# Optimization experiments

Measured on AMD Instinct MI355X. Metric: run time of the kernel, lower is better.

Reference implementation:

```python
import jax, jax.numpy as jnp
import numpy as np

B, N0, N1, FD, L, H = 4, 256, 256, 128, 3, 1
NG = N0 + N1            # nodes per graph
N = B * NG              # total nodes
EPS_BN = 1e-5
EPS_SM = 1e-16


def _build_edges():
    def perm_edges(n, off):
        idx = np.arange(n)
        a = np.repeat(idx, n); b = np.tile(idx, n)
        m = a != b
        return np.stack([a[m], b[m]]) + off
    e_intra = np.concatenate([perm_edges(N0, 0), perm_edges(N1, N0)], axis=1)
    a = np.arange(N0); b = np.arange(N0, N0 + N1)
    cross1 = np.stack([np.repeat(a, N1), np.tile(b, N0)])
    cross2 = np.stack([np.repeat(b, N0), np.tile(a, N1)])
    eg = np.concatenate([e_intra, cross1, cross2], axis=1)
    tg = np.concatenate([np.zeros(e_intra.shape[1], np.int32),
                         np.ones(cross1.shape[1] + cross2.shape[1], np.int32)])
    ei = np.concatenate([eg + g * NG for g in range(B)], axis=1).astype(np.int32)
    et = np.tile(tg, B).astype(np.int32)
    return jnp.asarray(ei), jnp.asarray(et)


def setup_inputs() -> dict:
    key = jax.random.key(0)
    ks = jax.random.split(key, 8)
    edge_index, edge_type = _build_edges()
    return {
        'desc0': jax.random.normal(ks[0], (B, FD, N0), jnp.float32),
        'desc1': jax.random.normal(ks[1], (B, FD, N1), jnp.float32),
        'W': jax.random.normal(ks[2], (L, 2, FD, H * FD), jnp.float32) * (1.0 / np.sqrt(FD)),
        'q': jax.random.normal(ks[3], (L, H * FD, H), jnp.float32) * 0.1,
        'k': jax.random.normal(ks[4], (L, H * FD, H), jnp.float32) * 0.1,
        'conv_b': jnp.zeros((L, FD), jnp.float32),
        'lin_W': jax.random.normal(ks[5], (L, FD, 2 * FD), jnp.float32) * (1.0 / np.sqrt(2 * FD)),
        'lin_b': jnp.zeros((L, FD), jnp.float32),
        'gamma': jnp.ones((L, FD), jnp.float32),
        'beta': jnp.zeros((L, FD), jnp.float32),
        'edge_index': edge_index,
        'edge_type': edge_type,
    }


def _forward(desc0, desc1, W, q, k, conv_b, lin_W, lin_b, gamma, beta, edge_index, edge_type):
    # x: [B, NG, FD] -> flattened batch graph [N, FD]
    x = jnp.concatenate([desc0, desc1], axis=2)        # [B, FD, NG]
    x = jnp.transpose(x, (0, 2, 1)).reshape(N, FD)
    src, dst = edge_index[0], edge_index[1]
    nlayers = W.shape[0]
    heads = q.shape[2]
    for l in range(nlayers):
        # relation-specific node projections (equiv to per-edge bmm with weight[edge_type])
        proj = jnp.einsum('nf,rfo->nro', x, W[l])       # [N, 2, H*FD]
        out_i = proj[dst, edge_type]                    # [E, H*FD]
        out_j = proj[src, edge_type]                    # [E, H*FD]
        alpha = jax.nn.leaky_relu(out_i @ q[l] + out_j @ k[l], 0.2)  # [E, H]
        # softmax over incoming edges of each destination node (across-relation)
        amax = jax.ops.segment_max(alpha, dst, num_segments=N)
        ex = jnp.exp(alpha - amax[dst])
        denom = jax.ops.segment_sum(ex, dst, num_segments=N)
        att = ex / (denom[dst] + EPS_SM)                # [E, H]
        msg = (att[:, :, None] * out_j.reshape(-1, heads, FD)).reshape(-1, heads * FD)
        agg = jax.ops.segment_sum(msg, dst, num_segments=N).reshape(N, heads, FD)
        m1 = jax.nn.relu(agg.mean(axis=1) + conv_b[l])  # concat=False -> mean over heads
        m2 = jnp.concatenate([x, m1], axis=1) @ lin_W[l].T + lin_b[l]
        mu = m2.mean(axis=0)
        var = ((m2 - mu) ** 2).mean(axis=0)             # biased var (BatchNorm training)
        m3 = (m2 - mu) / jnp.sqrt(var + EPS_BN) * gamma[l] + beta[l]
        x = x + m3
    x = x.reshape(B, NG, FD).transpose(0, 2, 1)         # [B, FD, NG]
    return x


def reference(desc0, desc1, W, q, k, conv_b, lin_W, lin_b, gamma, beta, edge_index, edge_type):
    x = _forward(desc0, desc1, W, q, k, conv_b, lin_W, lin_b, gamma, beta, edge_index, edge_type)
    return x[:, :, :N0], x[:, :, N0:]
```

## Files before the change

### kernel.cpp

```cpp
#include <hip/hip_runtime.h>

#define FD  128
#define NN  2048

#define OFF_X     0
#define OFF_PROJ  262144
#define OFF_QS    786432
#define OFF_KS    790528
#define OFF_SUMS  794624
#define OFF_LWT   800768
#define OFF_M2    899072

__device__ __forceinline__ int swizzle_n0(int bid) {
    int g    = (bid & 7) >> 1;
    int slot = ((bid >> 3) << 1) | (bid & 1);
    return g*512 + slot*4;
}

__device__ __forceinline__ void proj_qsks4(
    const float* __restrict__ W, const float* __restrict__ qv,
    const float* __restrict__ kv, float* __restrict__ ws,
    int l, int n0, int t, const float (*xs)[FD],
    float (*redp)[256], float* red)
{
    int kh = t >> 8, tp = t & 255;
    int rsel = tp >> 7, o = tp & 127;
    const float* Wl = W + ((size_t)(l*2 + rsel)*FD)*FD + o;
    float acc[4];
#pragma unroll
    for (int r = 0; r < 4; r++) acc[r] = 0.f;
    int kbase = kh * 64;
#pragma unroll
    for (int kk = 0; kk < 64; kk += 4) {
        int k4 = kbase + kk;
        float w0 = Wl[(k4+0)*FD], w1 = Wl[(k4+1)*FD];
        float w2 = Wl[(k4+2)*FD], w3 = Wl[(k4+3)*FD];
#pragma unroll
        for (int r = 0; r < 4; r++) {
            float4 xq = *(const float4*)&xs[r][k4];
            acc[r] += xq.x*w0 + xq.y*w1 + xq.z*w2 + xq.w*w3;
        }
    }
    if (kh == 1) {
#pragma unroll
        for (int r = 0; r < 4; r++) redp[r][tp] = acc[r];
    }
    __syncthreads();
    if (t < 256) {
#pragma unroll
        for (int r = 0; r < 4; r++) acc[r] += redp[r][tp];
#pragma unroll
        for (int r = 0; r < 4; r++)
            ws[OFF_PROJ + (size_t)(n0 + r)*256 + tp] = acc[r];

        float qq = qv[l*FD + o], kq = kv[l*FD + o];
        int lane = t & 63, w = t >> 6;
#pragma unroll
        for (int r = 0; r < 4; r++) {
            float vq = acc[r]*qq, vk = acc[r]*kq;
            for (int off = 32; off; off >>= 1) {
                vq += __shfl_xor(vq, off, 64);
                vk += __shfl_xor(vk, off, 64);
            }
            if (lane == 0) { red[w*8 + r*2] = vq; red[w*8 + r*2 + 1] = vk; }
        }
    }
    __syncthreads();
    if (t < 16) {
        int r = t & 3, rs = (t >> 2) & 1, wh = t >> 3;
        float v = red[(rs*2)*8 + r*2 + wh] + red[(rs*2 + 1)*8 + r*2 + wh];
        if (wh == 0) ws[OFF_QS + rs*NN + n0 + r] = v;
        else         ws[OFF_KS + rs*NN + n0 + r] = v;
    }
}

__global__ __launch_bounds__(512, 4) void k_pre(
    const float* __restrict__ d0, const float* __restrict__ d1,
    const float* __restrict__ W,  const float* __restrict__ qv,
    const float* __restrict__ kv, const float* __restrict__ linW,
    float* __restrict__ ws)
{
    int bid = blockIdx.x, t = threadIdx.x;
    if (bid >= 512) {
        if (bid < 536) {
            int vb = bid - 512;
#pragma unroll
            for (int i = 0; i < 8; i++) {
                int e = vb*4096 + i*512 + t;
                int l = e >> 15, rem = e & 32767;
                int o = rem >> 8, c = rem & 255;
                ws[OFF_LWT + l*32768 + c*FD + o] = linW[e];
            }
        } else {
            for (int i = t; i < 6144; i += 512) ws[OFF_SUMS + i] = 0.f;
        }
        return;
    }
    __shared__ __attribute__((aligned(16))) float xs[4][FD];
    __shared__ float redp[4][256];
    __shared__ float red[32];
    int n0 = swizzle_n0(bid);
    {
        int row = t >> 7, f = t & 127;
        int n = n0 + row, gg = n >> 9, ii = n & 511;
        float v = (ii < 256) ? d0[gg*32768 + f*256 + ii]
                             : d1[gg*32768 + f*256 + (ii - 256)];
        xs[row][f] = v;
        ws[OFF_X + (size_t)n*FD + f] = v;
    }
    __syncthreads();
    proj_qsks4(W, qv, kv, ws, 0, n0, t, xs, redp, red);
}

__global__ __launch_bounds__(512, 4) void k_bp(
    const float* __restrict__ W,     const float* __restrict__ qv,
    const float* __restrict__ kv,    const float* __restrict__ gamma,
    const float* __restrict__ beta,  float* __restrict__ ws, int l)
{
    __shared__ float scale[FD], shift[FD];
    __shared__ __attribute__((aligned(16))) float xs[4][FD];
    __shared__ float redp[4][256];
    __shared__ float red[32];
    int bid = blockIdx.x, t = threadIdx.x;
    int lp = l - 1;
    if (t < 128) {
        float s0 = 0.f, s1 = 0.f;
#pragma unroll
        for (int sl = 0; sl < 8; sl++) {
            s0 += ws[OFF_SUMS + lp*2048 + sl*256 + t];
            s1 += ws[OFF_SUMS + lp*2048 + sl*256 + 128 + t];
        }
        float mu  = s0 * (1.f/2048.f);
        float var = s1 * (1.f/2048.f) - mu*mu;
        float rs  = rsqrtf(var + 1e-5f);
        float gm  = gamma[lp*FD + t], bt = beta[lp*FD + t];
        scale[t] = gm * rs;
        shift[t] = bt - mu * gm * rs;
    }
    __syncthreads();
    int n0 = swizzle_n0(bid);
    {
        int row = t >> 7, f = t & 127;
        size_t e = (size_t)(n0 + row)*FD + f;
        float xv = ws[OFF_X + e] + ws[OFF_M2 + e]*scale[f] + shift[f];
        xs[row][f] = xv;
        ws[OFF_X + e] = xv;
    }
    __syncthreads();
    proj_qsks4(W, qv, kv, ws, l, n0, t, xs, redp, red);
}

__global__ __launch_bounds__(512, 4) void k_attn(
    const float* __restrict__ convb, const float* __restrict__ linb,
    float* __restrict__ ws, int l)
{
    __shared__ __attribute__((aligned(16))) float att[4*512];
    __shared__ __attribute__((aligned(16))) float redB[8*4*128];
    __shared__ __attribute__((aligned(16))) float cat[4*256];
    __shared__ float sml[4][2], sls[4][2];
    __shared__ float r1[FD], r2[FD];

    int bid = blockIdx.x, t = threadIdx.x;
    int dstbase = swizzle_n0(bid);
    int g = dstbase >> 9, dloc0 = dstbase & 511;
    int Gd = (dloc0 >= 256) ? 1 : 0;

    int f4 = t & 31, sq = t >> 5;
    int ts = (sq < 8) ? Gd : 1 - Gd;
    const float* P = ws + OFF_PROJ + (size_t)(g*512)*256 + ts*128 + f4*4;
    int s0 = sq * 32;
    float4 buf0[4], buf1[4], buf2[4];
#pragma unroll
    for (int u = 0; u < 4; u++) buf0[u] = *(const float4*)&P[(size_t)(s0+u)*256];
#pragma unroll
    for (int u = 0; u < 4; u++) buf1[u] = *(const float4*)&P[(size_t)(s0+4+u)*256];
    float xpre = ws[OFF_X + (size_t)(dstbase + (t >> 7))*FD + (t & 127)];
    float cb   = convb[l*FD + (t & 127)];
    float lb   = linb[l*FD + (t & 127)];

    {
        int w = t >> 6, p = t & 63;
        int d = w >> 1, h = w & 1;
        int dloc = dloc0 + d;
        float q0 = ws[OFF_QS + dstbase + d];
        float q1 = ws[OFF_QS + NN + dstbase + d];
        float sc[4];
#pragma unroll
        for (int j = 0; j < 4; j++) {
            int s = h*256 + p + j*64;
            int tss = (s < 256) ? Gd : 1 - Gd;
            float a = (tss ? q1 : q0) + ws[OFF_KS + tss*NN + g*512 + s];
            a = a > 0.f ? a : 0.2f*a;
            sc[j] = (s == dloc) ? -1e30f : a;
        }
        float lm = fmaxf(fmaxf(sc[0], sc[1]), fmaxf(sc[2], sc[3]));
        for (int off = 32; off; off >>= 1) lm = fmaxf(lm, __shfl_xor(lm, off, 64));
        float ex[4], lsum = 0.f;
#pragma unroll
        for (int j = 0; j < 4; j++) { ex[j] = __expf(sc[j] - lm); lsum += ex[j]; }
        for (int off = 32; off; off >>= 1) lsum += __shfl_xor(lsum, off, 64);
#pragma unroll
        for (int j = 0; j < 4; j++) att[d*512 + h*256 + p + j*64] = ex[j];
        if (p == 0) { sml[d][h] = lm; sls[d][h] = lsum; }
    }
    __syncthreads();
    {
        int d = t >> 7, s4 = (t & 127) * 4;
        int h = (s4 >= 256) ? 1 : 0;
        float m0 = sml[d][0], m1 = sml[d][1];
        float M = fmaxf(m0, m1);
        float denom = sls[d][0]*__expf(m0 - M) + sls[d][1]*__expf(m1 - M) + 1e-16f;
        float fac = __expf(sml[d][h] - M) / denom;
        float4 a4 = *(float4*)&att[d*512 + s4];
        a4.x *= fac; a4.y *= fac; a4.z *= fac; a4.w *= fac;
        *(float4*)&att[d*512 + s4] = a4;
        if (t < 128) r1[t] = 0.f;
        else if (t < 256) r2[t - 128] = 0.f;
    }
    __syncthreads();

    float acc[4][4];
#pragma unroll
    for (int d2 = 0; d2 < 4; d2++)
#pragma unroll
        for (int j = 0; j < 4; j++) acc[d2][j] = 0.f;
    {
#pragma unroll
        for (int ii = 0; ii < 8; ii++) {
            const float4* cur = (ii % 3 == 0) ? buf0 : (ii % 3 == 1) ? buf1 : buf2;
            float4* nxt = ((ii+2) % 3 == 0) ? buf0 : ((ii+2) % 3 == 1) ? buf1 : buf2;
            if (ii < 6) {
#pragma unroll
                for (int u = 0; u < 4; u++)
                    nxt[u] = *(const float4*)&P[(size_t)(s0 + (ii+2)*4 + u)*256];
            }
#pragma unroll
            for (int u = 0; u < 4; u++) {
                int s = s0 + ii*4 + u;
                float4 p4 = cur[u];
#pragma unroll
                for (int d2 = 0; d2 < 4; d2++) {
                    float b = att[d2*512 + s];
                    acc[d2][0] += b*p4.x; acc[d2][1] += b*p4.y;
                    acc[d2][2] += b*p4.z; acc[d2][3] += b*p4.w;
                }
            }
        }
    }
    if (sq >= 8) {
#pragma unroll
        for (int d2 = 0; d2 < 4; d2++)
            *(float4*)&redB[((sq - 8)*4 + d2)*128 + f4*4] =
                make_float4(acc[d2][0], acc[d2][1], acc[d2][2], acc[d2][3]);
    }
    __syncthreads();
    if (sq < 8) {
#pragma unroll
        for (int d2 = 0; d2 < 4; d2++) {
            float4 p4 = *(const float4*)&redB[(sq*4 + d2)*128 + f4*4];
            *(float4*)&redB[(sq*4 + d2)*128 + f4*4] =
                make_float4(acc[d2][0]+p4.x, acc[d2][1]+p4.y, acc[d2][2]+p4.z, acc[d2][3]+p4.w);
        }
    }
    __syncthreads();

    {
        int d2 = t >> 7, f = t & 127;
        float agg = 0.f;
#pragma unroll
        for (int cc = 0; cc < 8; cc++) agg += redB[(cc*4 + d2)*128 + f];
        float m1v = fmaxf(agg + cb, 0.f);
        cat[d2*256 + FD + f] = m1v;
        cat[d2*256 + f] = xpre;
    }
    __syncthreads();

#pragma unroll
    for (int d2 = 0; d2 < 4; d2++)
#pragma unroll
        for (int j = 0; j < 4; j++) acc[d2][j] = 0.f;
    {
        const float* lwt = ws + OFF_LWT + l*32768 + f4*4;
        int c0 = sq * 16;
#pragma unroll
        for (int u = 0; u < 4; u++) buf0[u] = *(const float4*)&lwt[(c0+u)*128];
#pragma unroll
        for (int u = 0; u < 4; u++) buf1[u] = *(const float4*)&lwt[(c0+4+u)*128];
#pragma unroll
        for (int ii = 0; ii < 4; ii++) {
            const float4* cur = (ii % 3 == 0) ? buf0 : (ii % 3 == 1) ? buf1 : buf2;
            float4* nxt = ((ii+2) % 3 == 0) ? buf0 : ((ii+2) % 3 == 1) ? buf1 : buf2;
            if (ii < 2) {
#pragma unroll
                for (int u = 0; u < 4; u++)
                    nxt[u] = *(const float4*)&lwt[(c0 + (ii+2)*4 + u)*128];
            }
#pragma unroll
            for (int u = 0; u < 4; u++) {
                int c = c0 + ii*4 + u;
                float4 w4 = cur[u];
#pragma unroll
                for (int d2 = 0; d2 < 4; d2++) {
                    float cv = cat[d2*256 + c];
                    acc[d2][0] += cv*w4.x; acc[d2][1] += cv*w4.y;
                    acc[d2][2] += cv*w4.z; acc[d2][3] += cv*w4.w;
                }
            }
        }
    }
    if (sq >= 8) {
#pragma unroll
        for (int d2 = 0; d2 < 4; d2++)
            *(float4*)&redB[((sq - 8)*4 + d2)*128 + f4*4] =
                make_float4(acc[d2][0], acc[d2][1], acc[d2][2], acc[d2][3]);
    }
    __syncthreads();
    if (sq < 8) {
#pragma unroll
        for (int d2 = 0; d2 < 4; d2++) {
            float4 p4 = *(const float4*)&redB[(sq*4 + d2)*128 + f4*4];
            *(float4*)&redB[(sq*4 + d2)*128 + f4*4] =
                make_float4(acc[d2][0]+p4.x, acc[d2][1]+p4.y, acc[d2][2]+p4.z, acc[d2][3]+p4.w);
        }
    }
    __syncthreads();

    {
        int d2 = t >> 7, o = t & 127;
        float m2v = lb;
#pragma unroll
        for (int cc = 0; cc < 8; cc++) m2v += redB[(cc*4 + d2)*128 + o];
        ws[OFF_M2 + (size_t)(dstbase + d2)*FD + o] = m2v;
        atomicAdd(&r1[o], m2v);
        atomicAdd(&r2[o], m2v*m2v);
    }
    __syncthreads();
    if (t < 128) {
        int slot = bid & 7;
        atomicAdd(&ws[OFF_SUMS + l*2048 + slot*256 + t],       r1[t]);
        atomicAdd(&ws[OFF_SUMS + l*2048 + slot*256 + 128 + t], r2[t]);
    }
}

__global__ __launch_bounds__(256) void k_bnout(
    const float* __restrict__ gamma, const float* __restrict__ beta,
    float* __restrict__ ws, float* __restrict__ out)
{
    __shared__ float scale[FD], shift[FD];
    int bid = blockIdx.x, t = threadIdx.x;
    if (t < 128) {
        float s0 = 0.f, s1 = 0.f;
#pragma unroll
        for (int sl = 0; sl < 8; sl++) {
            s0 += ws[OFF_SUMS + 2*2048 + sl*256 + t];
            s1 += ws[OFF_SUMS + 2*2048 + sl*256 + 128 + t];
        }
        float mu  = s0 * (1.f/2048.f);
        float var = s1 * (1.f/2048.f) - mu*mu;
        float rs  = rsqrtf(var + 1e-5f);
        float gm  = gamma[2*FD + t], bt = beta[2*FD + t];
        scale[t] = gm * rs;
        shift[t] = bt - mu * gm * rs;
    }
    __syncthreads();
#pragma unroll
    for (int i = 0; i < 2; i++) {
        int idx = bid*512 + i*256 + t;
        int f = idx & 127, n = idx >> 7;
        float v = ws[OFF_X + idx] + ws[OFF_M2 + idx]*scale[f] + shift[f];
        int gg = n >> 9, ii = n & 511;
        int off = (ii < 256) ? (gg*32768 + f*256 + ii)
                             : (131072 + gg*32768 + f*256 + (ii - 256));
        out[off] = v;
    }
}

extern "C" void kernel_launch(void* const* d_in, const int* in_sizes, int n_in,
                              void* d_out, int out_size, void* d_ws, size_t ws_size,
                              hipStream_t stream) {
    (void)in_sizes; (void)n_in; (void)out_size; (void)ws_size;
    const float* desc0 = (const float*)d_in[0];
    const float* desc1 = (const float*)d_in[1];
    const float* W     = (const float*)d_in[2];
    const float* q     = (const float*)d_in[3];
    const float* kk    = (const float*)d_in[4];
    const float* convb = (const float*)d_in[5];
    const float* linW  = (const float*)d_in[6];
    const float* linb  = (const float*)d_in[7];
    const float* gamma = (const float*)d_in[8];
    const float* beta  = (const float*)d_in[9];
    float* ws  = (float*)d_ws;
    float* out = (float*)d_out;

    hipLaunchKernelGGL(k_pre,  dim3(537), dim3(512), 0, stream, desc0, desc1, W, q, kk, linW, ws);
    hipLaunchKernelGGL(k_attn, dim3(512), dim3(512), 0, stream, convb, linb, ws, 0);
    hipLaunchKernelGGL(k_bp,   dim3(512), dim3(512), 0, stream, W, q, kk, gamma, beta, ws, 1);
    hipLaunchKernelGGL(k_attn, dim3(512), dim3(512), 0, stream, convb, linb, ws, 1);
    hipLaunchKernelGGL(k_bp,   dim3(512), dim3(512), 0, stream, W, q, kk, gamma, beta, ws, 2);
    hipLaunchKernelGGL(k_attn, dim3(512), dim3(512), 0, stream, convb, linb, ws, 2);
    hipLaunchKernelGGL(k_bnout, dim3(512), dim3(256), 0, stream, gamma, beta, ws, out);
}
```

Measured before the change: 153.4 us.

## Defer softmax normalization to accumulators, widen reduction buffer, hoist loads before barriers

The attention kernel no longer rescales the attention weights in shared memory in a separate pass. The per-half softmax factor is now applied to each thread's accumulators after the weighted sum. The two-step partial-sum reduction is replaced by all 16 groups writing to a doubled redB buffer, which removes several __syncthreads in both matmul phases. In k_bp and k_bnout, the global loads of x and m2 are hoisted above the BN-statistics barrier so their latency overlaps the stats computation. The cost is more shared memory per block, which could reduce occupancy, and a longer 16-way final sum.

```diff
diff --git a/kernel.cpp b/kernel.cpp
--- a/kernel.cpp
+++ b/kernel.cpp
@@ -123,6 +123,11 @@
     __shared__ float red[32];
     int bid = blockIdx.x, t = threadIdx.x;
     int lp = l - 1;
+    int n0 = swizzle_n0(bid);
+    int row = t >> 7, f = t & 127;
+    size_t e = (size_t)(n0 + row)*FD + f;
+    float xm  = ws[OFF_X + e];
+    float m2v = ws[OFF_M2 + e];
     if (t < 128) {
         float s0 = 0.f, s1 = 0.f;
 #pragma unroll
@@ -138,11 +143,8 @@
         shift[t] = bt - mu * gm * rs;
     }
     __syncthreads();
-    int n0 = swizzle_n0(bid);
-    {
-        int row = t >> 7, f = t & 127;
-        size_t e = (size_t)(n0 + row)*FD + f;
-        float xv = ws[OFF_X + e] + ws[OFF_M2 + e]*scale[f] + shift[f];
+    {
+        float xv = xm + m2v*scale[f] + shift[f];
         xs[row][f] = xv;
         ws[OFF_X + e] = xv;
     }
@@ -155,7 +157,7 @@
     float* __restrict__ ws, int l)
 {
     __shared__ __attribute__((aligned(16))) float att[4*512];
-    __shared__ __attribute__((aligned(16))) float redB[8*4*128];
+    __shared__ __attribute__((aligned(16))) float redB[16*4*128];
     __shared__ __attribute__((aligned(16))) float cat[4*256];
     __shared__ float sml[4][2], sls[4][2];
     __shared__ float r1[FD], r2[FD];
@@ -202,18 +204,8 @@
 #pragma unroll
         for (int j = 0; j < 4; j++) att[d*512 + h*256 + p + j*64] = ex[j];
         if (p == 0) { sml[d][h] = lm; sls[d][h] = lsum; }
-    }
-    __syncthreads();
-    {
-        int d = t >> 7, s4 = (t & 127) * 4;
-        int h = (s4 >= 256) ? 1 : 0;
-        float m0 = sml[d][0], m1 = sml[d][1];
-        float M = fmaxf(m0, m1);
-        float denom = sls[d][0]*__expf(m0 - M) + sls[d][1]*__expf(m1 - M) + 1e-16f;
-        float fac = __expf(sml[d][h] - M) / denom;
-        float4 a4 = *(float4*)&att[d*512 + s4];
-        a4.x *= fac; a4.y *= fac; a4.z *= fac; a4.w *= fac;
-        *(float4*)&att[d*512 + s4] = a4;
+        int d2 = t >> 7, f = t & 127;
+        cat[d2*256 + f] = xpre;
         if (t < 128) r1[t] = 0.f;
         else if (t < 256) r2[t - 128] = 0.f;
     }
@@ -246,21 +238,21 @@
                 }
             }
         }
-    }
-    if (sq >= 8) {
+        int h = (sq >= 8) ? 1 : 0;
+#pragma unroll
+        for (int d2 = 0; d2 < 4; d2++) {
+            float m0 = sml[d2][0], m1 = sml[d2][1];
+            float M = fmaxf(m0, m1);
+            float denom = sls[d2][0]*__expf(m0 - M) + sls[d2][1]*__expf(m1 - M)
+                        + 1e-16f;
+            float fac = __expf((h ? m1 : m0) - M) / denom;
+#pragma unroll
+            for (int j = 0; j < 4; j++) acc[d2][j] *= fac;
+        }
 #pragma unroll
         for (int d2 = 0; d2 < 4; d2++)
-            *(float4*)&redB[((sq - 8)*4 + d2)*128 + f4*4] =
+            *(float4*)&redB[(sq*4 + d2)*128 + f4*4] =
                 make_float4(acc[d2][0], acc[d2][1], acc[d2][2], acc[d2][3]);
-    }
-    __syncthreads();
-    if (sq < 8) {
-#pragma unroll
-        for (int d2 = 0; d2 < 4; d2++) {
-            float4 p4 = *(const float4*)&redB[(sq*4 + d2)*128 + f4*4];
-            *(float4*)&redB[(sq*4 + d2)*128 + f4*4] =
-                make_float4(acc[d2][0]+p4.x, acc[d2][1]+p4.y, acc[d2][2]+p4.z, acc[d2][3]+p4.w);
-        }
     }
     __syncthreads();
 
@@ -268,10 +260,8 @@
         int d2 = t >> 7, f = t & 127;
         float agg = 0.f;
 #pragma unroll
-        for (int cc = 0; cc < 8; cc++) agg += redB[(cc*4 + d2)*128 + f];
-        float m1v = fmaxf(agg + cb, 0.f);
-        cat[d2*256 + FD + f] = m1v;
-        cat[d2*256 + f] = xpre;
+        for (int cc = 0; cc < 16; cc++) agg += redB[(cc*4 + d2)*128 + f];
+        cat[d2*256 + FD + f] = fmaxf(agg + cb, 0.f);
     }
     __syncthreads();
 
@@ -307,21 +297,10 @@
                 }
             }
         }
-    }
-    if (sq >= 8) {
 #pragma unroll
         for (int d2 = 0; d2 < 4; d2++)
-            *(float4*)&redB[((sq - 8)*4 + d2)*128 + f4*4] =
+            *(float4*)&redB[(sq*4 + d2)*128 + f4*4] =
                 make_float4(acc[d2][0], acc[d2][1], acc[d2][2], acc[d2][3]);
-    }
-    __syncthreads();
-    if (sq < 8) {
-#pragma unroll
-        for (int d2 = 0; d2 < 4; d2++) {
-            float4 p4 = *(const float4*)&redB[(sq*4 + d2)*128 + f4*4];
-            *(float4*)&redB[(sq*4 + d2)*128 + f4*4] =
-                make_float4(acc[d2][0]+p4.x, acc[d2][1]+p4.y, acc[d2][2]+p4.z, acc[d2][3]+p4.w);
-        }
     }
     __syncthreads();
 
@@ -329,7 +308,7 @@
         int d2 = t >> 7, o = t & 127;
         float m2v = lb;
 #pragma unroll
-        for (int cc = 0; cc < 8; cc++) m2v += redB[(cc*4 + d2)*128 + o];
+        for (int cc = 0; cc < 16; cc++) m2v += redB[(cc*4 + d2)*128 + o];
         ws[OFF_M2 + (size_t)(dstbase + d2)*FD + o] = m2v;
         atomicAdd(&r1[o], m2v);
         atomicAdd(&r2[o], m2v*m2v);
@@ -348,6 +327,13 @@
 {
     __shared__ float scale[FD], shift[FD];
     int bid = blockIdx.x, t = threadIdx.x;
+    float xm[2], mm[2];
+#pragma unroll
+    for (int i = 0; i < 2; i++) {
+        int idx = bid*512 + i*256 + t;
+        xm[i] = ws[OFF_X + idx];
+        mm[i] = ws[OFF_M2 + idx];
+    }
     if (t < 128) {
         float s0 = 0.f, s1 = 0.f;
 #pragma unroll
@@ -367,7 +353,7 @@
     for (int i = 0; i < 2; i++) {
         int idx = bid*512 + i*256 + t;
         int f = idx & 127, n = idx >> 7;
-        float v = ws[OFF_X + idx] + ws[OFF_M2 + idx]*scale[f] + shift[f];
+        float v = xm[i] + mm[i]*scale[f] + shift[f];
         int gg = n >> 9, ii = n & 511;
         int off = (ii < 256) ? (gg*32768 + f*256 + ii)
                              : (131072 + gg*32768 + f*256 + (ii - 256));
```

Result: no change. 154.9 us (+0.9%).
